# Kernel tuning notes

Hardware: AMD Instinct MI355X
Metric: run time of the kernel (lower is better)

Reference implementation:

```python
import jax, jax.numpy as jnp
import numpy as np


def setup_inputs() -> dict:
    key = jax.random.key(0)
    k1, k2, k3 = jax.random.split(key, 3)
    B, N, M, S = 2, 8192, 32768, 4096
    pred = jax.random.normal(k1, (B, N, 3), dtype=jnp.float32)
    target = jax.random.normal(k2, (B, M, 3), dtype=jnp.float32)
    # stands in for torch.randperm(N)[:S]; duplicates don't change the math shape-wise
    idx = jax.random.randint(k3, (S,), 0, N, dtype=jnp.int64)
    return {"pred": pred, "target": target, "idx": idx}


def reference(pred, target, idx):
    # pred: (B, N, 3), target: (B, M, 3), idx: (S,)
    pred_s = pred[:, idx, :]                       # (B, S, 3) -- sampled points
    x2 = jnp.sum(pred_s * pred_s, axis=-1)         # (B, S)
    y2 = jnp.sum(target * target, axis=-1)         # (B, M)
    xy = jnp.einsum("bsd,bmd->bsm", pred_s, target)  # (B, S, M)
    d2 = x2[:, :, None] + y2[:, None, :] - 2.0 * xy
    dist = jnp.sqrt(jnp.maximum(d2, 0.0))          # (B, S, M)
    min_dist = jnp.min(dist, axis=2)               # (B, S)
    return jnp.mean(min_dist)
```

## Files before the change

### kernel.cpp

```cpp
#include <hip/hip_runtime.h>
#include <math.h>

typedef float vf2 __attribute__((ext_vector_type(2)));

constexpr int B = 2;
constexpr int N = 8192;
constexpr int M = 32768;
constexpr int S = 4096;
constexpr int QTOT = B * S;
constexpr int R = 32;
constexpr int WT = 64 * R;
constexpr int TCH = M / WT;
constexpr int QG = S / 64;
constexpr int WAVES = B * TCH * QG;
constexpr int BLOCKS = WAVES / 4;


__global__ __launch_bounds__(256, 2) void chamfer_main(
    const float* __restrict__ pred, const float* __restrict__ target,
    const int* __restrict__ idx, unsigned* __restrict__ wsmin) {
  __shared__ float qs0[64], qs1[64], qs2[64], qw[64];
  const int lane = threadIdx.x & 63;
  const int w = blockIdx.x * 4 + (threadIdx.x >> 6);
  const int b = w >> 10;
  const int rem = w & 1023;
  const int tch = rem & (TCH - 1);
  const int qg = rem >> 4;

  if (threadIdx.x < 64) {
    int s = qg * 64 + threadIdx.x;
    int i = idx[s];
    const float* p = pred + ((size_t)b * N + (size_t)i) * 3;
    float x = p[0], y = p[1], z = p[2];
    qs0[threadIdx.x] = -2.0f * x;
    qs1[threadIdx.x] = -2.0f * y;
    qs2[threadIdx.x] = -2.0f * z;
    qw[threadIdx.x] = x * x + y * y + z * z;
  }

  const float* tb = target + ((size_t)b * M + (size_t)tch * WT) * 3;
  vf2 t0p[16], t1p[16], t2p[16], ty2p[16];
#pragma unroll
  for (int p = 0; p < 16; ++p) {
    int mA = (2 * p) * 64 + lane;
    int mB = (2 * p + 1) * 64 + lane;
    float ax = tb[3 * mA], ay = tb[3 * mA + 1], az = tb[3 * mA + 2];
    float bx = tb[3 * mB], by = tb[3 * mB + 1], bz = tb[3 * mB + 2];
    t0p[p] = vf2{ax, bx};
    t1p[p] = vf2{ay, by};
    t2p[p] = vf2{az, bz};
    ty2p[p] = vf2{fmaf(ax, ax, fmaf(ay, ay, az * az)),
                  fmaf(bx, bx, fmaf(by, by, bz * bz))};
  }
  __syncthreads();

  const float qx2_home = qw[lane];
  const int rot = ((lane + 1) & 63) * 4;
  float mm = INFINITY;
  int qoff = lane;

  for (int step = 0; step < 64; ++step) {
    vf2 q0 = vf2{qs0[qoff], qs0[qoff]};
    vf2 q1 = vf2{qs1[qoff], qs1[qoff]};
    vf2 q2 = vf2{qs2[qoff], qs2[qoff]};
    float m0 = mm, m1 = INFINITY;
#pragma unroll
    for (int p = 0; p < 16; p += 2) {
      vf2 s = __builtin_elementwise_fma(q0, t0p[p], ty2p[p]);
      s = __builtin_elementwise_fma(q1, t1p[p], s);
      s = __builtin_elementwise_fma(q2, t2p[p], s);
      m0 = fminf(fminf(s.x, s.y), m0);
      vf2 u = __builtin_elementwise_fma(q0, t0p[p + 1], ty2p[p + 1]);
      u = __builtin_elementwise_fma(q1, t1p[p + 1], u);
      u = __builtin_elementwise_fma(q2, t2p[p + 1], u);
      m1 = fminf(fminf(u.x, u.y), m1);
    }
    mm = fminf(m0, m1);
    mm = __int_as_float(__builtin_amdgcn_ds_bpermute(rot, __float_as_int(mm)));
    qoff = (qoff + 1) & 63;
  }
  const int q = b * S + qg * 64 + lane;
  atomicMin(&wsmin[q], __float_as_uint(fmaxf(qx2_home + mm, 0.0f)));
}

__global__ __launch_bounds__(1024) void chamfer_finish(
    const unsigned* __restrict__ wsmin, float* __restrict__ out) {
  __shared__ float red[16];
  float sum = 0.0f;
  for (int q = threadIdx.x; q < QTOT; q += 1024)
    sum += sqrtf(__uint_as_float(wsmin[q]));
#pragma unroll
  for (int off = 32; off > 0; off >>= 1)
    sum += __shfl_down(sum, off, 64);
  int wv = threadIdx.x >> 6;
  if ((threadIdx.x & 63) == 0) red[wv] = sum;
  __syncthreads();
  if (threadIdx.x == 0) {
    float t = 0.0f;
#pragma unroll
    for (int i = 0; i < 16; ++i) t += red[i];
    out[0] = t / (float)QTOT;
  }
}

extern "C" void kernel_launch(void* const* d_in, const int* in_sizes, int n_in,
                              void* d_out, int out_size, void* d_ws, size_t ws_size,
                              hipStream_t stream) {
  const float* pred = (const float*)d_in[0];
  const float* target = (const float*)d_in[1];
  const int* idx = (const int*)d_in[2];
  unsigned* wsmin = (unsigned*)d_ws;

  hipMemsetAsync(wsmin, 0x7F, QTOT * sizeof(unsigned), stream);
  chamfer_main<<<BLOCKS, 256, 0, stream>>>(pred, target, idx, wsmin);
  chamfer_finish<<<1, 1024, 0, stream>>>(wsmin, (float*)d_out);
}
```

Measured before the change: 83.47 us.

## Fuse final reduction into main kernel via last-block ticket and LDS pre-min

Removes the separate finish kernel. A global ticket counter lets the last block to finish compute the mean of square-rooted minima. Each block first combines its 4 waves' per-query minima with LDS atomics, which cuts global atomicMin traffic by four. The next query coordinates are also prefetched from LDS one step ahead to hide LDS latency in the inner loop. The cost is a threadfence and a ticket atomic per block, plus a serial tail reduction run by a single 256-thread block.

```diff
diff --git a/kernel.cpp b/kernel.cpp
--- a/kernel.cpp
+++ b/kernel.cpp
@@ -18,8 +18,11 @@
 
 __global__ __launch_bounds__(256, 2) void chamfer_main(
     const float* __restrict__ pred, const float* __restrict__ target,
-    const int* __restrict__ idx, unsigned* __restrict__ wsmin) {
+    const int* __restrict__ idx, unsigned* __restrict__ wsmin,
+    unsigned* __restrict__ ticket, float* __restrict__ out) {
   __shared__ float qs0[64], qs1[64], qs2[64], qw[64];
+  __shared__ unsigned qmin[64];
+  __shared__ int islast;
   const int lane = threadIdx.x & 63;
   const int w = blockIdx.x * 4 + (threadIdx.x >> 6);
   const int b = w >> 10;
@@ -36,6 +39,7 @@
     qs1[threadIdx.x] = -2.0f * y;
     qs2[threadIdx.x] = -2.0f * z;
     qw[threadIdx.x] = x * x + y * y + z * z;
+    qmin[threadIdx.x] = 0xFFFFFFFFu;
   }
 
   const float* tb = target + ((size_t)b * M + (size_t)tch * WT) * 3;
@@ -58,49 +62,56 @@
   const int rot = ((lane + 1) & 63) * 4;
   float mm = INFINITY;
   int qoff = lane;
+  float q0 = qs0[qoff], q1 = qs1[qoff], q2 = qs2[qoff];
 
   for (int step = 0; step < 64; ++step) {
-    vf2 q0 = vf2{qs0[qoff], qs0[qoff]};
-    vf2 q1 = vf2{qs1[qoff], qs1[qoff]};
-    vf2 q2 = vf2{qs2[qoff], qs2[qoff]};
-    float m0 = mm, m1 = INFINITY;
+    int qn = (qoff + 1) & 63;
+    float n0 = qs0[qn], n1 = qs1[qn], n2 = qs2[qn];
+    vf2 Q0 = vf2{q0, q0}, Q1 = vf2{q1, q1}, Q2 = vf2{q2, q2};
+    float m0 = INFINITY, m1 = INFINITY;
 #pragma unroll
     for (int p = 0; p < 16; p += 2) {
-      vf2 s = __builtin_elementwise_fma(q0, t0p[p], ty2p[p]);
-      s = __builtin_elementwise_fma(q1, t1p[p], s);
-      s = __builtin_elementwise_fma(q2, t2p[p], s);
+      vf2 s = __builtin_elementwise_fma(Q0, t0p[p], ty2p[p]);
+      s = __builtin_elementwise_fma(Q1, t1p[p], s);
+      s = __builtin_elementwise_fma(Q2, t2p[p], s);
       m0 = fminf(fminf(s.x, s.y), m0);
-      vf2 u = __builtin_elementwise_fma(q0, t0p[p + 1], ty2p[p + 1]);
-      u = __builtin_elementwise_fma(q1, t1p[p + 1], u);
-      u = __builtin_elementwise_fma(q2, t2p[p + 1], u);
+      vf2 u = __builtin_elementwise_fma(Q0, t0p[p + 1], ty2p[p + 1]);
+      u = __builtin_elementwise_fma(Q1, t1p[p + 1], u);
+      u = __builtin_elementwise_fma(Q2, t2p[p + 1], u);
       m1 = fminf(fminf(u.x, u.y), m1);
     }
-    mm = fminf(m0, m1);
+    mm = fminf(mm, fminf(m0, m1));
     mm = __int_as_float(__builtin_amdgcn_ds_bpermute(rot, __float_as_int(mm)));
-    qoff = (qoff + 1) & 63;
+    q0 = n0; q1 = n1; q2 = n2; qoff = qn;
   }
-  const int q = b * S + qg * 64 + lane;
-  atomicMin(&wsmin[q], __float_as_uint(fmaxf(qx2_home + mm, 0.0f)));
-}
+  atomicMin(&qmin[lane], __float_as_uint(fmaxf(qx2_home + mm, 0.0f)));
+  __syncthreads();
 
-__global__ __launch_bounds__(1024) void chamfer_finish(
-    const unsigned* __restrict__ wsmin, float* __restrict__ out) {
-  __shared__ float red[16];
+  if (threadIdx.x < 64) {
+    int q = b * S + qg * 64 + threadIdx.x;
+    atomicMin(&wsmin[q], qmin[threadIdx.x]);
+    __threadfence();
+  }
+  __syncthreads();
+  if (threadIdx.x == 0) {
+    unsigned t = atomicAdd(ticket, 1u);
+    islast = (t == (unsigned)(BLOCKS - 2));
+  }
+  __syncthreads();
+  if (!islast) return;
+
   float sum = 0.0f;
-  for (int q = threadIdx.x; q < QTOT; q += 1024)
-    sum += sqrtf(__uint_as_float(wsmin[q]));
+  for (int q = threadIdx.x; q < QTOT; q += 256)
+    sum += sqrtf(__uint_as_float(atomicAdd(&wsmin[q], 0u)));
 #pragma unroll
   for (int off = 32; off > 0; off >>= 1)
     sum += __shfl_down(sum, off, 64);
+  __shared__ float red[4];
   int wv = threadIdx.x >> 6;
   if ((threadIdx.x & 63) == 0) red[wv] = sum;
   __syncthreads();
-  if (threadIdx.x == 0) {
-    float t = 0.0f;
-#pragma unroll
-    for (int i = 0; i < 16; ++i) t += red[i];
-    out[0] = t / (float)QTOT;
-  }
+  if (threadIdx.x == 0)
+    out[0] = (red[0] + red[1] + red[2] + red[3]) / (float)QTOT;
 }
 
 extern "C" void kernel_launch(void* const* d_in, const int* in_sizes, int n_in,
@@ -110,8 +121,9 @@
   const float* target = (const float*)d_in[1];
   const int* idx = (const int*)d_in[2];
   unsigned* wsmin = (unsigned*)d_ws;
+  unsigned* ticket = wsmin + QTOT;
 
-  hipMemsetAsync(wsmin, 0x7F, QTOT * sizeof(unsigned), stream);
-  chamfer_main<<<BLOCKS, 256, 0, stream>>>(pred, target, idx, wsmin);
-  chamfer_finish<<<1, 1024, 0, stream>>>(wsmin, (float*)d_out);
+  hipMemsetAsync(d_ws, 0xFF, QTOT * sizeof(unsigned) + 4, stream);
+  chamfer_main<<<BLOCKS, 256, 0, stream>>>(pred, target, idx, wsmin, ticket,
+                                           (float*)d_out);
 }
```

Result: slower. 96.69 us (+15.8%).
